# Performance work log

Measured on AMD Instinct MI355X. Metric: run time of the kernel, lower is better.

## Reference

```python
import jax, jax.numpy as jnp
import numpy as np

DIM = 1024


def _combine(e1, e2):
    # associative op for h_t = a_t * h_{t-1} + b_t (inclusive scan, h_0-contrib handled outside)
    a1, b1 = e1
    a2, b2 = e2
    return a1 * a2, b2 + a2 * b1


def setup_inputs() -> dict:
    key = jax.random.key(0)
    ks = jax.random.split(key, 11)
    s = 1.0 / np.sqrt(DIM)
    d = {
        "x": jax.random.normal(ks[0], (4, 4096, DIM), jnp.float32),
        "hidden": jax.random.normal(ks[1], (4, DIM), jnp.float32),
        "Wf": jax.random.uniform(ks[2], (DIM, DIM), jnp.float32, -s, s),
        "bf": jax.random.uniform(ks[3], (DIM,), jnp.float32, -s, s),
        "Wi": jax.random.uniform(ks[4], (DIM, DIM), jnp.float32, -s, s),
        "bi": jax.random.uniform(ks[5], (DIM,), jnp.float32, -s, s),
        "Wig": jax.random.uniform(ks[6], (DIM, DIM), jnp.float32, -s, s),
        "big": jax.random.uniform(ks[7], (DIM,), jnp.float32, -s, s),
        "Wog": jax.random.uniform(ks[8], (DIM, DIM), jnp.float32, -s, s),
        "bog": jax.random.uniform(ks[9], (DIM,), jnp.float32, -s, s),
    }
    return d


def reference(x, hidden, Wf, bf, Wi, bi, Wig, big, Wog, bog):
    # x: [B, L, D], hidden: [B, D]
    forget = jax.nn.sigmoid(jnp.einsum("bld,ed->ble", x, Wf) + bf)
    inp = jnp.tanh(jnp.einsum("bld,ed->ble", x, Wi) + bi) * \
          jax.nn.sigmoid(jnp.einsum("bld,ed->ble", x, Wig) + big)
    # parallel scan of h_t = forget_t * h_{t-1} + inp_t with h_0 = 0
    _, h_inner = jax.lax.associative_scan(_combine, (forget, inp), axis=1)
    # add initial-hidden contribution: hidden * prod_{s<=t} forget_s
    h = h_inner + hidden[:, None, :] * jnp.cumprod(forget, axis=1)
    y = jnp.tanh(h) * jax.nn.sigmoid(jnp.einsum("bld,ed->ble", x, Wog) + bog)
    return y, h[:, -1, :]
```

## Files before the change

### kernel.cpp

```cpp
#include <hip/hip_runtime.h>
#include <hip/hip_bf16.h>
#include <cstdint>
#include <cstddef>

#define DIMD 1024
#define LSEQ 4096
#define BATCH 4
#define MTOT (BATCH*LSEQ)
#define NCHUNK 64
#define CHUNKLEN 64
#define GATE_ELEMS ((size_t)MTOT*DIMD)
#define NTILE_K 32

typedef __bf16 bf16x8 __attribute__((ext_vector_type(8)));
typedef float f32x4 __attribute__((ext_vector_type(4)));

__device__ __forceinline__ unsigned short f2bf(float f) {
    union { float f; uint32_t u; } v; v.f = f;
    uint32_t r = v.u + 0x7fffu + ((v.u >> 16) & 1u);
    return (unsigned short)(r >> 16);
}
__device__ __forceinline__ float bits2f(unsigned short b) {
    union { uint32_t u; float f; } v; v.u = ((uint32_t)b) << 16; return v.f;
}
__device__ __forceinline__ float gld(const float* p, size_t o) { return p[o]; }
__device__ __forceinline__ float gld(const unsigned short* p, size_t o) { return bits2f(p[o]); }
__device__ __forceinline__ void  gst(float* p, size_t o, float v) { p[o] = v; }
__device__ __forceinline__ void  gst(unsigned short* p, size_t o, float v) { p[o] = f2bf(v); }

__device__ __forceinline__ float fsig(float x) {
    return __builtin_amdgcn_rcpf(1.f + __expf(-x));
}

__global__ void cast_f32_to_bf16(const float* __restrict__ src,
                                 unsigned short* __restrict__ dst, int n) {
    int i = (blockIdx.x * blockDim.x + threadIdx.x) * 8;
    if (i >= n) return;
    float4 a = *(const float4*)(src + i);
    float4 b = *(const float4*)(src + i + 4);
    uint4 o;
    o.x = (uint32_t)f2bf(a.x) | ((uint32_t)f2bf(a.y) << 16);
    o.y = (uint32_t)f2bf(a.z) | ((uint32_t)f2bf(a.w) << 16);
    o.z = (uint32_t)f2bf(b.x) | ((uint32_t)f2bf(b.y) << 16);
    o.w = (uint32_t)f2bf(b.z) | ((uint32_t)f2bf(b.w) << 16);
    *(uint4*)(dst + i) = o;
}

template <typename T>
__global__ __launch_bounds__(512, 4) void gemm_gates_s(
    const unsigned short* __restrict__ Xb,
    const unsigned short* __restrict__ Wcat,
    const float* __restrict__ bf_, const float* __restrict__ bi_,
    const float* __restrict__ big_, const float* __restrict__ bog_,
    T* __restrict__ G)
{
    __shared__ __align__(16) char lds[73728];
    char* ldsA = lds;
    char* ldsB = lds + 24576;

    const int tid = threadIdx.x;
    const int wave = tid >> 6, lane = tid & 63;
    const int wm = wave >> 2, wn = wave & 3;
    const int l15 = lane & 15, l4 = lane >> 4;

    const int wg = blockIdx.x;
    const int swz = (wg & 7) * 256 + (wg >> 3);
    const int mt = swz & 127, nt = swz >> 7;
    const int m0 = mt * 128, n0 = nt * 256;

    const int rsw = (l4 ^ (l15 & 3)) << 4;
    const char* ArdBase = ldsA + (wm * 64 + l15) * 64 + rsw;
    const char* BrdBase = ldsB + (wn * 64 + l15) * 64 + rsw;

    const int srow = tid >> 2;
    const int scg  = ((tid & 3) ^ (srow & 3)) * 8;
    const unsigned short* pAsrc  = Xb   + (size_t)(m0 + srow) * DIMD + scg;
    const unsigned short* pBsrc0 = Wcat + (size_t)(n0 + srow) * DIMD + scg;
    const unsigned short* pBsrc1 = Wcat + (size_t)(n0 + 128 + srow) * DIMD + scg;

    auto stage3 = [&](int k0, int offA, int offB) {
        __builtin_amdgcn_global_load_lds(
            (const __attribute__((address_space(1))) uint32_t*)(pAsrc + k0),
            (__attribute__((address_space(3))) uint32_t*)(ldsA + offA + (wave << 10)), 16, 0, 0);
        __builtin_amdgcn_global_load_lds(
            (const __attribute__((address_space(1))) uint32_t*)(pBsrc0 + k0),
            (__attribute__((address_space(3))) uint32_t*)(ldsB + offB + (wave << 10)), 16, 0, 0);
        __builtin_amdgcn_global_load_lds(
            (const __attribute__((address_space(1))) uint32_t*)(pBsrc1 + k0),
            (__attribute__((address_space(3))) uint32_t*)(ldsB + offB + 8192 + (wave << 10)), 16, 0, 0);
    };

    f32x4 acc[4][4];
#pragma unroll
    for (int m = 0; m < 4; ++m)
#pragma unroll
        for (int n = 0; n < 4; ++n) acc[m][n] = (f32x4)0.f;

    stage3(0, 0, 0);
    stage3(32, 8192, 16384);

    int offA0 = 0, offA1 = 8192, offA2 = 16384;
    int offB0 = 0, offB1 = 16384, offB2 = 32768;
#pragma unroll 1
    for (int t = 0; t < NTILE_K; ++t) {
        if (t <= NTILE_K - 2) asm volatile("s_waitcnt vmcnt(3)" ::: "memory");
        else                  asm volatile("s_waitcnt vmcnt(0)" ::: "memory");
        __builtin_amdgcn_s_barrier();
        __builtin_amdgcn_sched_barrier(0);

        if (t + 2 < NTILE_K) stage3((t + 2) * 32, offA2, offB2);

        bf16x8 bv[4], avl[2], avh[2];
#pragma unroll
        for (int n = 0; n < 4; ++n)
            bv[n] = *(const bf16x8*)(BrdBase + offB0 + n * 1024);
        avl[0] = *(const bf16x8*)(ArdBase + offA0);
        avl[1] = *(const bf16x8*)(ArdBase + offA0 + 1024);

        __builtin_amdgcn_s_setprio(1);
#pragma unroll
        for (int m = 0; m < 2; ++m)
#pragma unroll
            for (int n = 0; n < 4; ++n)
                acc[m][n] = __builtin_amdgcn_mfma_f32_16x16x32_bf16(avl[m], bv[n], acc[m][n], 0, 0, 0);
        __builtin_amdgcn_s_setprio(0);

        avh[0] = *(const bf16x8*)(ArdBase + offA0 + 2048);
        avh[1] = *(const bf16x8*)(ArdBase + offA0 + 3072);

        __builtin_amdgcn_s_setprio(1);
#pragma unroll
        for (int m = 0; m < 2; ++m)
#pragma unroll
            for (int n = 0; n < 4; ++n)
                acc[2 + m][n] = __builtin_amdgcn_mfma_f32_16x16x32_bf16(avh[m], bv[n], acc[2 + m][n], 0, 0, 0);
        __builtin_amdgcn_s_setprio(0);

        int ta = offA0; offA0 = offA1; offA1 = offA2; offA2 = ta;
        int tb = offB0; offB0 = offB1; offB1 = offB2; offB2 = tb;
    }

    const int gate = n0 >> 10;
    const float* bias = (gate == 0) ? bf_ : (gate == 1) ? bi_ : (gate == 2) ? big_ : bog_;
    T* Gg = G + (size_t)gate * GATE_ELEMS;
    const int ebase = (n0 & 1023) + wn * 64;
    const int rowb0 = m0 + wm * 64;
    float bvv[4];
#pragma unroll
    for (int nf = 0; nf < 4; ++nf) bvv[nf] = bias[ebase + nf * 16 + l15];
#pragma unroll
    for (int mf = 0; mf < 4; ++mf) {
        int rowb = rowb0 + mf * 16 + l4 * 4;
#pragma unroll
        for (int r = 0; r < 4; ++r) {
            size_t rowoff = (size_t)(rowb + r) * DIMD;
#pragma unroll
            for (int nf = 0; nf < 4; ++nf) {
                float pre = acc[mf][nf][r] + bvv[nf];
                float v = (gate == 1) ? (2.f * fsig(2.f * pre) - 1.f) : fsig(pre);
                gst(Gg, rowoff + ebase + nf * 16 + l15, v);
            }
        }
    }
}

template <typename T>
__global__ void scan_phase1(const T* __restrict__ F, const T* __restrict__ TI,
                            const T* __restrict__ SG,
                            float* __restrict__ Aagg, float* __restrict__ Bagg) {
    const int d = blockIdx.x * blockDim.x + threadIdx.x;
    const int c = blockIdx.y, b = blockIdx.z;
    size_t base = ((size_t)b * LSEQ + (size_t)c * CHUNKLEN) * DIMD + d;
    float A = 1.f, Bv = 0.f;
#pragma unroll 8
    for (int t = 0; t < CHUNKLEN; ++t) {
        size_t off = base + (size_t)t * DIMD;
        float f = gld(F, off);
        float i = gld(TI, off) * gld(SG, off);
        A *= f;
        Bv = __builtin_fmaf(f, Bv, i);
    }
    size_t o = ((size_t)b * NCHUNK + c) * DIMD + d;
    Aagg[o] = A;
    Bagg[o] = Bv;
}

__global__ void scan_phase2(const float* __restrict__ Aagg, const float* __restrict__ Bagg,
                            const float* __restrict__ hidden,
                            float* __restrict__ Hstart, float* __restrict__ out_h) {
    int idx = blockIdx.x * blockDim.x + threadIdx.x;
    int b = idx >> 10, d = idx & 1023;
    float h = hidden[b * 1024 + d];
    for (int c = 0; c < NCHUNK; ++c) {
        size_t o = ((size_t)b * NCHUNK + c) * DIMD + d;
        Hstart[o] = h;
        h = __builtin_fmaf(Aagg[o], h, Bagg[o]);
    }
    out_h[b * 1024 + d] = h;
}

template <typename T>
__global__ void scan_phase3(const T* __restrict__ F, const T* __restrict__ TI,
                            const T* __restrict__ SG, const T* __restrict__ OG,
                            const float* __restrict__ Hstart, float* __restrict__ y) {
    const int d = blockIdx.x * blockDim.x + threadIdx.x;
    const int c = blockIdx.y, b = blockIdx.z;
    float h = Hstart[((size_t)b * NCHUNK + c) * DIMD + d];
    size_t base = ((size_t)b * LSEQ + (size_t)c * CHUNKLEN) * DIMD + d;
#pragma unroll 4
    for (int t = 0; t < CHUNKLEN; ++t) {
        size_t off = base + (size_t)t * DIMD;
        float f = gld(F, off);
        float i = gld(TI, off) * gld(SG, off);
        h = __builtin_fmaf(f, h, i);
        y[off] = tanhf(h) * gld(OG, off);
    }
}

extern "C" void kernel_launch(void* const* d_in, const int* in_sizes, int n_in,
                              void* d_out, int out_size, void* d_ws, size_t ws_size,
                              hipStream_t stream) {
    const float* x      = (const float*)d_in[0];
    const float* hidden = (const float*)d_in[1];
    const float* Wf  = (const float*)d_in[2];
    const float* bf_ = (const float*)d_in[3];
    const float* Wi  = (const float*)d_in[4];
    const float* bi_ = (const float*)d_in[5];
    const float* Wig = (const float*)d_in[6];
    const float* big_= (const float*)d_in[7];
    const float* Wog = (const float*)d_in[8];
    const float* bog_= (const float*)d_in[9];

    char* ws = (char*)d_ws;
    unsigned short* Xb   = (unsigned short*)(ws);
    unsigned short* Wcat = (unsigned short*)(ws + 33554432);

    float* y     = (float*)d_out;
    float* out_h = y + GATE_ELEMS;

    cast_f32_to_bf16<<<MTOT * DIMD / 8 / 256, 256, 0, stream>>>(x, Xb, MTOT * DIMD);
    cast_f32_to_bf16<<<DIMD * DIMD / 8 / 256, 256, 0, stream>>>(Wf,  Wcat + 0 * DIMD * DIMD, DIMD * DIMD);
    cast_f32_to_bf16<<<DIMD * DIMD / 8 / 256, 256, 0, stream>>>(Wi,  Wcat + 1 * DIMD * DIMD, DIMD * DIMD);
    cast_f32_to_bf16<<<DIMD * DIMD / 8 / 256, 256, 0, stream>>>(Wig, Wcat + 2 * DIMD * DIMD, DIMD * DIMD);
    cast_f32_to_bf16<<<DIMD * DIMD / 8 / 256, 256, 0, stream>>>(Wog, Wcat + 3 * DIMD * DIMD, DIMD * DIMD);

    const int GRID = (MTOT / 128) * (4096 / 256);
    const size_t FP32_WS_NEED = 33554432ull + 8388608ull + GATE_ELEMS * 4 * 4 + 3ull * 1048576ull;
    if (ws_size >= FP32_WS_NEED) {
        float* G      = (float*)(ws + 41943040);
        float* Aagg   = (float*)(ws + 310378496);
        float* Bagg   = (float*)(ws + 311427072);
        float* Hstart = (float*)(ws + 312475648);
        gemm_gates_s<float><<<GRID, 512, 0, stream>>>(Xb, Wcat, bf_, bi_, big_, bog_, G);
        const float* Fg  = G;
        const float* TIg = G + 1 * GATE_ELEMS;
        const float* SGg = G + 2 * GATE_ELEMS;
        const float* OGg = G + 3 * GATE_ELEMS;
        scan_phase1<float><<<dim3(DIMD / 256, NCHUNK, BATCH), 256, 0, stream>>>(Fg, TIg, SGg, Aagg, Bagg);
        scan_phase2<<<BATCH * DIMD / 256, 256, 0, stream>>>(Aagg, Bagg, hidden, Hstart, out_h);
        scan_phase3<float><<<dim3(DIMD / 256, NCHUNK, BATCH), 256, 0, stream>>>(Fg, TIg, SGg, OGg, Hstart, y);
    } else {
        unsigned short* G = (unsigned short*)(ws + 41943040);
        float* Aagg   = (float*)(ws + 176160768);
        float* Bagg   = (float*)(ws + 177209344);
        float* Hstart = (float*)(ws + 178257920);
        gemm_gates_s<unsigned short><<<GRID, 512, 0, stream>>>(Xb, Wcat, bf_, bi_, big_, bog_, G);
        const unsigned short* Fg  = G;
        const unsigned short* TIg = G + 1 * GATE_ELEMS;
        const unsigned short* SGg = G + 2 * GATE_ELEMS;
        const unsigned short* OGg = G + 3 * GATE_ELEMS;
        scan_phase1<unsigned short><<<dim3(DIMD / 256, NCHUNK, BATCH), 256, 0, stream>>>(Fg, TIg, SGg, Aagg, Bagg);
        scan_phase2<<<BATCH * DIMD / 256, 256, 0, stream>>>(Aagg, Bagg, hidden, Hstart, out_h);
        scan_phase3<unsigned short><<<dim3(DIMD / 256, NCHUNK, BATCH), 256, 0, stream>>>(Fg, TIg, SGg, OGg, Hstart, y);
    }
}
```

Baseline: 250.5 us.

## Merge cast kernels into one launch and change LDS swizzle pattern

Folds the five separate fp32-to-bf16 cast launches into a single kernel that maps block ranges to x and the four weight matrices. This removes per-launch overhead and the tail gaps between the small weight casts. It also changes the XOR swizzle used for LDS staging and reads in the GEMM from row&3 to (row>>1)&3, aiming to reduce LDS bank conflicts for the 64-byte row stride. The write-side and read-side swizzles must stay consistent, and they were changed together.

```diff
diff --git a/kernel.cpp b/kernel.cpp
--- a/kernel.cpp
+++ b/kernel.cpp
@@ -32,17 +32,27 @@
     return __builtin_amdgcn_rcpf(1.f + __expf(-x));
 }
 
-__global__ void cast_f32_to_bf16(const float* __restrict__ src,
-                                 unsigned short* __restrict__ dst, int n) {
-    int i = (blockIdx.x * blockDim.x + threadIdx.x) * 8;
-    if (i >= n) return;
+__global__ void cast_all(const float* __restrict__ x,
+                         const float* __restrict__ Wf, const float* __restrict__ Wi,
+                         const float* __restrict__ Wig, const float* __restrict__ Wog,
+                         unsigned short* __restrict__ Xb, unsigned short* __restrict__ Wcat) {
+    int b = blockIdx.x;
+    const float* src; unsigned short* dst; int lb;
+    if (b < 8192) { src = x; dst = Xb; lb = b; }
+    else {
+        int w = (b - 8192) >> 9;
+        lb = (b - 8192) & 511;
+        src = (w == 0) ? Wf : (w == 1) ? Wi : (w == 2) ? Wig : Wog;
+        dst = Wcat + (size_t)w * DIMD * DIMD;
+    }
+    int i = (lb * 256 + threadIdx.x) * 8;
     float4 a = *(const float4*)(src + i);
-    float4 b = *(const float4*)(src + i + 4);
+    float4 c = *(const float4*)(src + i + 4);
     uint4 o;
     o.x = (uint32_t)f2bf(a.x) | ((uint32_t)f2bf(a.y) << 16);
     o.y = (uint32_t)f2bf(a.z) | ((uint32_t)f2bf(a.w) << 16);
-    o.z = (uint32_t)f2bf(b.x) | ((uint32_t)f2bf(b.y) << 16);
-    o.w = (uint32_t)f2bf(b.z) | ((uint32_t)f2bf(b.w) << 16);
+    o.z = (uint32_t)f2bf(c.x) | ((uint32_t)f2bf(c.y) << 16);
+    o.w = (uint32_t)f2bf(c.z) | ((uint32_t)f2bf(c.w) << 16);
     *(uint4*)(dst + i) = o;
 }
 
@@ -68,12 +78,12 @@
     const int mt = swz & 127, nt = swz >> 7;
     const int m0 = mt * 128, n0 = nt * 256;
 
-    const int rsw = (l4 ^ (l15 & 3)) << 4;
+    const int rsw = (l4 ^ ((l15 >> 1) & 3)) << 4;
     const char* ArdBase = ldsA + (wm * 64 + l15) * 64 + rsw;
     const char* BrdBase = ldsB + (wn * 64 + l15) * 64 + rsw;
 
     const int srow = tid >> 2;
-    const int scg  = ((tid & 3) ^ (srow & 3)) * 8;
+    const int scg  = ((tid & 3) ^ ((srow >> 1) & 3)) * 8;
     const unsigned short* pAsrc  = Xb   + (size_t)(m0 + srow) * DIMD + scg;
     const unsigned short* pBsrc0 = Wcat + (size_t)(n0 + srow) * DIMD + scg;
     const unsigned short* pBsrc1 = Wcat + (size_t)(n0 + 128 + srow) * DIMD + scg;
@@ -238,11 +248,7 @@
     float* y     = (float*)d_out;
     float* out_h = y + GATE_ELEMS;
 
-    cast_f32_to_bf16<<<MTOT * DIMD / 8 / 256, 256, 0, stream>>>(x, Xb, MTOT * DIMD);
-    cast_f32_to_bf16<<<DIMD * DIMD / 8 / 256, 256, 0, stream>>>(Wf,  Wcat + 0 * DIMD * DIMD, DIMD * DIMD);
-    cast_f32_to_bf16<<<DIMD * DIMD / 8 / 256, 256, 0, stream>>>(Wi,  Wcat + 1 * DIMD * DIMD, DIMD * DIMD);
-    cast_f32_to_bf16<<<DIMD * DIMD / 8 / 256, 256, 0, stream>>>(Wig, Wcat + 2 * DIMD * DIMD, DIMD * DIMD);
-    cast_f32_to_bf16<<<DIMD * DIMD / 8 / 256, 256, 0, stream>>>(Wog, Wcat + 3 * DIMD * DIMD, DIMD * DIMD);
+    cast_all<<<10240, 256, 0, stream>>>(x, Wf, Wi, Wig, Wog, Xb, Wcat);
 
     const int GRID = (MTOT / 128) * (4096 / 256);
     const size_t FP32_WS_NEED = 33554432ull + 8388608ull + GATE_ELEMS * 4 * 4 + 3ull * 1048576ull;
```

New measurement: 240.4 us. 1.04x faster.
